# Kernel tuning notes

Measured on AMD Instinct MI355X. Metric: run time of the kernel, lower is better.

Reference implementation:

```python
import jax, jax.numpy as jnp
import numpy as np
from jax import lax

DN = ('NCHW', 'OIHW', 'NCHW')
DENSITY = 0.1  # fraction of active pillar sites


def conv(x, w, stride=1):
    return lax.conv_general_dilated(x, w, (stride, stride), ((1, 1), (1, 1)), dimension_numbers=DN)


def bn(x, s, t):
    # inference-mode BN folded into per-channel scale/shift
    return x * s[None, :, None, None] + t[None, :, None, None]


def subm(x, w, s, t, mask):
    # submanifold sparse conv == dense conv on zero-filled grid, outputs kept only at active sites
    return bn(conv(x, w), s, t) * mask


def basic_block(x, mask, w, s, t):
    # Sparse2DBasicBlock: relu(bn(conv)) -> bn(conv) -> add identity -> relu
    out = jax.nn.relu(subm(x, w[0], s[0], t[0], mask))
    out = subm(out, w[1], s[1], t[1], mask)
    return jax.nn.relu(out + x)


def downsample_mask(m):
    # regular sparse conv (k=3, s=2, p=1): output active iff any input in window active
    return lax.reduce_window(m, 0.0, lax.max, (1, 1, 3, 3), (1, 1, 2, 2), ((0, 0), (0, 0), (1, 1), (1, 1)))


def down_stage(x, m_in, wd, w, s, t):
    m = downsample_mask(m_in)
    h = jax.nn.relu(bn(conv(x, wd, 2), s[0], t[0]) * m)
    h = basic_block(h, m, w[0:2], s[1:3], t[1:3])
    h = basic_block(h, m, w[2:4], s[3:5], t[3:5])
    return h, m


def forward_all(x, mask, w1, s1, t1, wd2, w2, s2, t2, wd3, w3, s3, t3, wd4, w4, s4, t4, w5, s5, t5):
    x = x * mask
    # conv1: Sparse2DBasicBlockV (conv0 + block) + Sparse2DBasicBlock
    h = jax.nn.relu(subm(x, w1[0], s1[0], t1[0], mask))
    h = basic_block(h, mask, w1[1:3], s1[1:3], t1[1:3])
    x1 = basic_block(h, mask, w1[3:5], s1[3:5], t1[3:5])
    x2, m2 = down_stage(x1, mask, wd2, w2, s2, t2)
    x3, m3 = down_stage(x2, m2, wd3, w3, s3, t3)
    x4, m4 = down_stage(x3, m3, wd4, w4, s4, t4)
    # conv5: dense stage on x_conv4.dense()
    h = jax.nn.relu(bn(conv(x4, w5[0], 2), s5[0], t5[0]))
    h = jax.nn.relu(bn(conv(h, w5[1]), s5[1], t5[1]))
    x5 = jax.nn.relu(bn(conv(h, w5[2]), s5[2], t5[2]))
    return x1, x2, x3, x4, x5


def setup_inputs() -> dict:
    key = jax.random.key(0)
    ks = jax.random.split(key, 16)
    B, C, H, W = 2, 32, 512, 512

    def mkw(k, o, i, n=None):
        shape = (o, i, 3, 3) if n is None else (n, o, i, 3, 3)
        return jax.random.normal(k, shape, jnp.float32) * float(np.sqrt(2.0 / (i * 9)))

    def sb(k, n, c):
        k1, k2 = jax.random.split(k)
        return (1.0 + 0.1 * jax.random.normal(k1, (n, c), jnp.float32),
                0.05 * jax.random.normal(k2, (n, c), jnp.float32))

    x = jax.random.normal(ks[0], (B, C, H, W), jnp.float32)
    mask_p = jax.random.uniform(ks[1], (B, 1, H, W), jnp.float32)
    w1 = mkw(ks[2], 32, 32, 5); s1, t1 = sb(ks[3], 5, 32)
    wd2 = mkw(ks[4], 64, 32); w2 = mkw(ks[5], 64, 64, 4); s2, t2 = sb(ks[6], 5, 64)
    wd3 = mkw(ks[7], 128, 64); w3 = mkw(ks[8], 128, 128, 4); s3, t3 = sb(ks[9], 5, 128)
    wd4 = mkw(ks[10], 256, 128); w4 = mkw(ks[11], 256, 256, 4); s4, t4 = sb(ks[12], 5, 256)
    w5 = mkw(ks[13], 256, 256, 3); s5, t5 = sb(ks[14], 3, 256)
    return dict(x=x, mask_p=mask_p, w1=w1, s1=s1, t1=t1, wd2=wd2, w2=w2, s2=s2, t2=t2,
                wd3=wd3, w3=w3, s3=s3, t3=t3, wd4=wd4, w4=w4, s4=s4, t4=t4,
                w5=w5, s5=s5, t5=t5)


def reference(x, mask_p, w1, s1, t1, wd2, w2, s2, t2, wd3, w3, s3, t3, wd4, w4, s4, t4, w5, s5, t5):
    mask = (mask_p < DENSITY).astype(x.dtype)
    return forward_all(x, mask, w1, s1, t1, wd2, w2, s2, t2, wd3, w3, s3, t3, wd4, w4, s4, t4, w5, s5, t5)
```

## Files before the change

### kernel.cpp

```cpp
#include <hip/hip_runtime.h>

typedef __attribute__((ext_vector_type(8))) _Float16 f16x8;
typedef __attribute__((ext_vector_type(4))) _Float16 f16x4;
typedef __attribute__((ext_vector_type(4))) float f32x4;

__global__ void mask_make(const float* __restrict__ x, const float* __restrict__ mp,
                          float* __restrict__ m, _Float16* __restrict__ x0,
                          int* __restrict__ act, int* __restrict__ cnt,
                          int B, int HW) {
    int i = blockIdx.x * blockDim.x + threadIdx.x;
    const int tid = threadIdx.x;
    const int lane = tid & 63;
    const int wv = tid >> 6;
    bool active = (mp[i] < 0.1f);
    float mv = active ? 1.0f : 0.0f;
    m[i] = mv;
    int b = i / HW, p = i - b * HW;
    const float* xb = x + ((size_t)b * 32) * HW + p;
    _Float16* ob = x0 + (size_t)i * 32;
    #pragma unroll
    for (int c = 0; c < 32; ++c) ob[c] = (_Float16)(xb[(size_t)c * HW] * mv);

    __shared__ int wcnt[4];
    __shared__ int bbase;
    unsigned long long ball = __ballot(active);
    int wtot = __popcll(ball);
    int prefix = __popcll(ball & ((1ull << lane) - 1ull));
    if (lane == 0) wcnt[wv] = wtot;
    __syncthreads();
    if (tid == 0) {
        int s = 0;
        #pragma unroll
        for (int w = 0; w < 4; ++w) { int tv = wcnt[w]; wcnt[w] = s; s += tv; }
        bbase = (s > 0) ? atomicAdd(&cnt[b], s) : 0;
    }
    __syncthreads();
    if (active) act[b * HW + bbase + wcnt[wv] + prefix] = p;
}

__global__ void mask_down(const float* __restrict__ mi, float* __restrict__ mo,
                          int B, int Hi, int Wi, int Ho, int Wo) {
    int i = blockIdx.x * blockDim.x + threadIdx.x;
    if (i >= B * Ho * Wo) return;
    int wo = i % Wo;
    int t = i / Wo;
    int ho = t % Ho;
    int b = t / Ho;
    float v = 0.0f;
    #pragma unroll
    for (int kh = 0; kh < 3; ++kh) {
        int hi = ho * 2 + kh - 1;
        if (hi < 0 || hi >= Hi) continue;
        #pragma unroll
        for (int kw = 0; kw < 3; ++kw) {
            int wi = wo * 2 + kw - 1;
            if (wi < 0 || wi >= Wi) continue;
            v = fmaxf(v, mi[((size_t)b * Hi + hi) * Wi + wi]);
        }
    }
    mo[i] = v;
}

struct WSeg { const float* src; int cin, cout, ck, cum; };
struct WArgs { WSeg seg[23]; int total; };

__global__ void reorder_all(WArgs A, _Float16* __restrict__ rw) {
    int idx = blockIdx.x * 256 + threadIdx.x;
    if (idx >= A.total) return;
    int s = 0;
    #pragma unroll
    for (int k = 1; k < 23; ++k) if (idx >= A.seg[k].cum) s = k;
    WSeg g = A.seg[s];
    int local = idx - g.cum;
    int kk = local % g.ck;
    int t2 = local / g.ck;
    int co = t2 % g.cout;
    int chunk = t2 / g.cout;
    int chunkc = g.cin / g.ck;
    int tap = chunk / chunkc, cc = chunk - tap * chunkc;
    int ci = cc * g.ck + kk;
    rw[g.cum + local] = (_Float16)g.src[((size_t)co * g.cin + ci) * 9 + tap];
}

template<int BM, int BN, int CK>
__global__ __launch_bounds__(256, 4)
void conv_mfma(const _Float16* __restrict__ in, const _Float16* __restrict__ rw,
               const float* __restrict__ s, const float* __restrict__ t,
               const float* __restrict__ mask, const _Float16* __restrict__ res,
               float* __restrict__ out32, _Float16* __restrict__ out16,
               int Cin, int Cout, int Hin, int Win, int Hout, int Wout,
               int TH, int TW, int stride, int relu)
{
    constexpr int WM = BM / 2;
    constexpr int WAVES_N = 2;
    constexpr int WN = BN / WAVES_N;
    constexpr int MR = WM / 16;
    constexpr int NR = WN / 16;
    constexpr int KH = CK / 32;
    constexpr int ELEMS = (CK * BN) / 256;
    constexpr int NV = ELEMS / 8;
    constexpr int TPP = 256 / BN;
    constexpr int LDST = CK + 8;

    __shared__ _Float16 Bsm[2][BN * LDST];

    const int tid = threadIdx.x;
    const int lane = tid & 63;
    const int wv = tid >> 6;
    const int wm = wv >> 1;
    const int wn = wv & 1;
    const int row = lane & 15, q = lane >> 4;

    const int tilesX = Wout / TW;
    const int oy0 = (blockIdx.x / tilesX) * TH;
    const int ox0 = (blockIdx.x % tilesX) * TW;
    const int co0 = blockIdx.y * BM;
    const int b = blockIdx.z;

    const int HWin = Hin * Win;
    const int HWo = Hout * Wout;
    const int cicn = Cin >> 5;
    const int cocn = Cout >> 5;
    const int chunkc = Cin / CK;
    const int nIter = 9 * chunkc;

    const int sn = tid / TPP;
    const int kb = (tid % TPP) * ELEMS;
    const int sty = sn / TW;
    const int stx = sn - sty * TW;
    const int soy = oy0 + sty;
    const int sox = ox0 + stx;

    f32x4 acc[MR][NR];
    #pragma unroll
    for (int m = 0; m < MR; ++m)
        #pragma unroll
        for (int n = 0; n < NR; ++n)
            #pragma unroll
            for (int r = 0; r < 4; ++r) acc[m][n][r] = 0.0f;

    auto LOADG = [&](int c, f16x8* dst) {
        int tap = c / chunkc, cc = c - tap * chunkc;
        int iy = soy * stride + (tap / 3) - 1;
        int ix = sox * stride + (tap - (tap / 3) * 3) - 1;
        bool ok = (iy >= 0 && iy < Hin && ix >= 0 && ix < Win);
        size_t pixoff = (size_t)iy * Win + ix;
        #pragma unroll
        for (int i = 0; i < NV; ++i) {
            int k = kb + 8 * i;
            const _Float16* p = in +
                (((size_t)(b * cicn + cc * KH + (k >> 5)) * HWin + pixoff) << 5) + (k & 31);
            dst[i] = ok ? *(const f16x8*)p : f16x8{};
        }
    };
    auto LOADW = [&](int c, f16x8 (&dst)[KH][MR]) {
        #pragma unroll
        for (int m = 0; m < MR; ++m) {
            int co = co0 + wm * WM + m * 16 + row;
            const _Float16* ap = rw + ((size_t)c * Cout + co) * CK + (q << 3);
            #pragma unroll
            for (int h = 0; h < KH; ++h) dst[h][m] = *(const f16x8*)(ap + 32 * h);
        }
    };
    auto WLDS = [&](int buf, const f16x8* v) {
        #pragma unroll
        for (int i = 0; i < NV; ++i)
            *(f16x8*)&Bsm[buf][sn * LDST + kb + 8 * i] = v[i];
    };
    auto DO_CHUNK = [&](const _Float16* bp, f16x8 (&awx)[KH][MR]) {
        f16x8 bh[KH][NR];
        #pragma unroll
        for (int n = 0; n < NR; ++n) {
            int nl = wn * WN + n * 16 + row;
            const _Float16* bb = bp + nl * LDST + (q << 3);
            #pragma unroll
            for (int h = 0; h < KH; ++h) bh[h][n] = *(const f16x8*)(bb + 32 * h);
        }
        #pragma unroll
        for (int h = 0; h < KH; ++h)
            #pragma unroll
            for (int m = 0; m < MR; ++m)
                #pragma unroll
                for (int n = 0; n < NR; ++n)
                    acc[m][n] = __builtin_amdgcn_mfma_f32_16x16x32_f16(awx[h][m], bh[h][n], acc[m][n], 0, 0, 0);
    };

    f16x8 awA[KH][MR], awB[KH][MR];
    f16x8 v[NV];
    LOADG(0, v);
    LOADW(0, awA);
    WLDS(0, v);
    __syncthreads();

    for (int c = 0; c < nIter; c += 2) {
        f16x8 v2[NV];
        bool h1 = (c + 1) < nIter;
        if (h1) { LOADG(c + 1, v2); LOADW(c + 1, awB); }
        DO_CHUNK(&Bsm[0][0], awA);
        if (h1) WLDS(1, v2);
        __syncthreads();
        if (!h1) break;
        f16x8 v3[NV];
        bool h2 = (c + 2) < nIter;
        if (h2) { LOADG(c + 2, v3); LOADW(c + 2, awA); }
        DO_CHUNK(&Bsm[1][0], awB);
        if (h2) WLDS(0, v3);
        __syncthreads();
    }

    int pix[NR]; float mv[NR];
    #pragma unroll
    for (int n = 0; n < NR; ++n) {
        int nl = wn * WN + n * 16 + row;
        int ty = nl / TW, tx = nl - ty * TW;
        pix[n] = (oy0 + ty) * Wout + (ox0 + tx);
        mv[n] = mask ? mask[(size_t)b * HWo + pix[n]] : 1.0f;
    }
    #pragma unroll
    for (int m = 0; m < MR; ++m) {
        int cb = co0 + wm * WM + m * 16 + q * 4;
        float sc[4], sh[4];
        #pragma unroll
        for (int r = 0; r < 4; ++r) { sc[r] = s[cb + r]; sh[r] = t[cb + r]; }
        #pragma unroll
        for (int n = 0; n < NR; ++n) {
            size_t boff = ((size_t)(b * cocn + (cb >> 5)) * HWo + pix[n]) * 32 + (cb & 31);
            float val[4];
            #pragma unroll
            for (int r = 0; r < 4; ++r) val[r] = (acc[m][n][r] * sc[r] + sh[r]) * mv[n];
            if (res) {
                f16x4 rv = *(const f16x4*)&res[boff];
                #pragma unroll
                for (int r = 0; r < 4; ++r) val[r] += (float)rv[r];
            }
            if (relu) {
                #pragma unroll
                for (int r = 0; r < 4; ++r) val[r] = fmaxf(val[r], 0.0f);
            }
            if (out16) {
                f16x4 pk;
                #pragma unroll
                for (int r = 0; r < 4; ++r) pk[r] = (_Float16)val[r];
                *(f16x4*)&out16[boff] = pk;
            }
            if (out32) {
                #pragma unroll
                for (int r = 0; r < 4; ++r)
                    out32[((size_t)b * Cout + cb + r) * HWo + pix[n]] = val[r];
            }
        }
    }
}

__global__ __launch_bounds__(256, 4)
void conv_bf(const _Float16* __restrict__ in, const _Float16* __restrict__ rw,
             const float* __restrict__ s, const float* __restrict__ t,
             const float* __restrict__ mask, const _Float16* __restrict__ res,
             float* __restrict__ out32, _Float16* __restrict__ out16,
             int Cin, int Cout, int Hin, int Win, int Hout, int Wout,
             int stride, int relu)
{
    const int lane = threadIdx.x & 63;
    const int wv = threadIdx.x >> 6;
    const int row = lane & 15, q = lane >> 4;
    const int b = blockIdx.z;
    const int HWo = Hout * Wout;
    const int ntile = HWo >> 4;
    const int gw = blockIdx.x * 4 + wv;
    const int tile = gw % ntile;
    const int cog = gw / ntile;
    const int co0 = cog * 64;
    const int HWin = Hin * Win;
    const int cicn = Cin >> 5;
    const int cocn = Cout >> 5;
    const int nIter = 9 * cicn;

    const int pix = tile * 16 + row;
    const int py = pix / Wout, px_ = pix - py * Wout;
    const int iy0 = py * stride - 1, ix0 = px_ * stride - 1;
    const _Float16* inb = in + (((size_t)b * cicn) * HWin << 5);

    f32x4 acc[4];
    #pragma unroll
    for (int m = 0; m < 4; ++m)
        #pragma unroll
        for (int r = 0; r < 4; ++r) acc[m][r] = 0.0f;

    auto LOADB = [&](int c, f16x8& dst) {
        int tap = c / cicn, cc = c - tap * cicn;
        int iy = iy0 + tap / 3, ix = ix0 + tap - (tap / 3) * 3;
        bool ok = (iy >= 0 && iy < Hin && ix >= 0 && ix < Win);
        dst = ok ? *(const f16x8*)(inb + (((size_t)cc * HWin + (size_t)iy * Win + ix) << 5) + (q << 3))
                 : f16x8{};
    };
    auto LOADA = [&](int c, f16x8 (&dst)[4]) {
        const _Float16* ap = rw + ((size_t)c * Cout + co0 + row) * 32 + (q << 3);
        #pragma unroll
        for (int m = 0; m < 4; ++m) dst[m] = *(const f16x8*)(ap + (size_t)m * 512);
    };

    f16x8 aA[4], aB[4], bfA, bfB;
    LOADB(0, bfA); LOADA(0, aA);
    for (int c = 0; c < nIter; c += 2) {
        bool h1 = (c + 1) < nIter, h2 = (c + 2) < nIter;
        if (h1) { LOADB(c + 1, bfB); LOADA(c + 1, aB); }
        #pragma unroll
        for (int m = 0; m < 4; ++m)
            acc[m] = __builtin_amdgcn_mfma_f32_16x16x32_f16(aA[m], bfA, acc[m], 0, 0, 0);
        if (h2) { LOADB(c + 2, bfA); LOADA(c + 2, aA); }
        if (h1) {
            #pragma unroll
            for (int m = 0; m < 4; ++m)
                acc[m] = __builtin_amdgcn_mfma_f32_16x16x32_f16(aB[m], bfB, acc[m], 0, 0, 0);
        }
    }

    float mv = mask ? mask[(size_t)b * HWo + pix] : 1.0f;
    #pragma unroll
    for (int m = 0; m < 4; ++m) {
        int cb = co0 + m * 16 + q * 4;
        size_t boff = ((size_t)(b * cocn + (cb >> 5)) * HWo + pix) * 32 + (cb & 31);
        float val[4];
        #pragma unroll
        for (int r = 0; r < 4; ++r) val[r] = (acc[m][r] * s[cb + r] + t[cb + r]) * mv;
        if (res) {
            f16x4 rv = *(const f16x4*)&res[boff];
            #pragma unroll
            for (int r = 0; r < 4; ++r) val[r] += (float)rv[r];
        }
        if (relu) {
            #pragma unroll
            for (int r = 0; r < 4; ++r) val[r] = fmaxf(val[r], 0.0f);
        }
        if (out16) {
            f16x4 pk;
            #pragma unroll
            for (int r = 0; r < 4; ++r) pk[r] = (_Float16)val[r];
            *(f16x4*)&out16[boff] = pk;
        }
        if (out32) {
            #pragma unroll
            for (int r = 0; r < 4; ++r)
                out32[((size_t)b * Cout + cb + r) * HWo + pix] = val[r];
        }
    }
}

__global__ __launch_bounds__(256, 4)
void conv_sparse(const _Float16* __restrict__ in, const _Float16* __restrict__ rw,
                 const float* __restrict__ s, const float* __restrict__ t,
                 const int* __restrict__ act, const int* __restrict__ cnt,
                 const _Float16* __restrict__ res,
                 float* __restrict__ out32, _Float16* __restrict__ out16,
                 int Hin, int Win, int relu)
{
    const int tid = threadIdx.x;
    const int lane = tid & 63;
    const int wv = tid >> 6;
    const int row = lane & 15, q = lane >> 4;
    const int b = blockIdx.z;
    const int HW = Hin * Win;
    const int nb = cnt[b];
    const int base = (blockIdx.x * 4 + wv) * 16;
    if (base >= nb) return;

    const int* actb = act + b * HW;
    const _Float16* inb = in + ((size_t)b * HW << 5);

    int j = base + row;
    bool vn = j < nb;
    int pn = vn ? actb[j] : 0;
    int py = pn / Win, px = pn - py * Win;

    f32x4 acc0, acc1;
    #pragma unroll
    for (int r = 0; r < 4; ++r) { acc0[r] = 0.0f; acc1[r] = 0.0f; }

    #pragma unroll
    for (int c = 0; c < 9; ++c) {
        const int dy = c / 3 - 1, dx = c - (c / 3) * 3 - 1;
        f16x8 a0 = *(const f16x8*)(rw + ((size_t)c * 32 + row) * 32 + (q << 3));
        f16x8 a1 = *(const f16x8*)(rw + ((size_t)c * 32 + 16 + row) * 32 + (q << 3));
        int iy = py + dy, ix = px + dx;
        bool ok = vn && iy >= 0 && iy < Hin && ix >= 0 && ix < Win;
        f16x8 bf = ok ? *(const f16x8*)(inb + ((size_t)(iy * Win + ix) << 5) + (q << 3))
                      : f16x8{};
        acc0 = __builtin_amdgcn_mfma_f32_16x16x32_f16(a0, bf, acc0, 0, 0, 0);
        acc1 = __builtin_amdgcn_mfma_f32_16x16x32_f16(a1, bf, acc1, 0, 0, 0);
    }

    if (!vn) return;
    size_t pbase = ((size_t)b * HW + pn) << 5;
    #pragma unroll
    for (int m = 0; m < 2; ++m) {
        const f32x4& am = m ? acc1 : acc0;
        int cb = m * 16 + q * 4;
        float val[4];
        #pragma unroll
        for (int r = 0; r < 4; ++r) val[r] = am[r] * s[cb + r] + t[cb + r];
        if (res) {
            f16x4 rv = *(const f16x4*)&res[pbase + cb];
            #pragma unroll
            for (int r = 0; r < 4; ++r) val[r] += (float)rv[r];
        }
        if (relu) {
            #pragma unroll
            for (int r = 0; r < 4; ++r) val[r] = fmaxf(val[r], 0.0f);
        }
        f16x4 pk;
        #pragma unroll
        for (int r = 0; r < 4; ++r) pk[r] = (_Float16)val[r];
        *(f16x4*)&out16[pbase + cb] = pk;
        if (out32) {
            #pragma unroll
            for (int r = 0; r < 4; ++r)
                out32[((size_t)(b * 32 + cb + r)) * HW + pn] = val[r];
        }
    }
}

extern "C" void kernel_launch(void* const* d_in, const int* in_sizes, int n_in,
                              void* d_out, int out_size, void* d_ws, size_t ws_size,
                              hipStream_t stream) {
    const int B = 2;

    const float* x      = (const float*)d_in[0];
    const float* mask_p = (const float*)d_in[1];
    const float* w1  = (const float*)d_in[2];
    const float* s1  = (const float*)d_in[3];
    const float* t1  = (const float*)d_in[4];
    const float* wd2 = (const float*)d_in[5];
    const float* w2  = (const float*)d_in[6];
    const float* s2  = (const float*)d_in[7];
    const float* t2  = (const float*)d_in[8];
    const float* wd3 = (const float*)d_in[9];
    const float* w3  = (const float*)d_in[10];
    const float* s3  = (const float*)d_in[11];
    const float* t3  = (const float*)d_in[12];
    const float* wd4 = (const float*)d_in[13];
    const float* w4  = (const float*)d_in[14];
    const float* s4  = (const float*)d_in[15];
    const float* t4  = (const float*)d_in[16];
    const float* w5  = (const float*)d_in[17];
    const float* s5  = (const float*)d_in[18];
    const float* t5  = (const float*)d_in[19];

    float* x1o = (float*)d_out;
    float* x2o = x1o + 16777216;
    float* x3o = x2o + 8388608;
    float* x4o = x3o + 4194304;
    float* x5o = x4o + 2097152;

    _Float16* rwbase = (_Float16*)d_ws;
    float* m1 = (float*)d_ws + 2649600;
    float* m2 = m1 + 524288;
    float* m3 = m2 + 131072;
    float* m4 = m3 + 32768;
    int* act  = (int*)(m4 + 8192);
    int* cnt  = act + 524288;
    _Float16* P = (_Float16*)(cnt + 32);
    _Float16* Q = P + 16777216;
    _Float16* R = Q + 16777216;

    WArgs wa;
    int cum = 0, si = 0;
    const _Float16* rp[23];
    auto addseg = [&](const float* src, int cin, int cout, int ck) {
        wa.seg[si].src = src; wa.seg[si].cin = cin; wa.seg[si].cout = cout;
        wa.seg[si].ck = ck; wa.seg[si].cum = cum;
        rp[si] = rwbase + cum;
        cum += cout * cin * 9; si++;
    };
    for (int i = 0; i < 5; ++i) addseg(w1 + (size_t)i * 9216, 32, 32, 32);
    addseg(wd2, 32, 64, 32);
    for (int i = 0; i < 4; ++i) addseg(w2 + (size_t)i * 36864, 64, 64, 64);
    addseg(wd3, 64, 128, 64);
    for (int i = 0; i < 4; ++i) addseg(w3 + (size_t)i * 147456, 128, 128, 64);
    addseg(wd4, 128, 256, 32);
    for (int i = 0; i < 4; ++i) addseg(w4 + (size_t)i * 589824, 256, 256, 32);
    for (int i = 0; i < 3; ++i) addseg(w5 + (size_t)i * 589824, 256, 256, 32);
    wa.total = cum;
    reorder_all<<<(cum + 255) / 256, 256, 0, stream>>>(wa, rwbase);

    hipMemsetAsync(cnt, 0, 2 * sizeof(int), stream);
    hipMemsetAsync(Q, 0, 2 * 16777216 * sizeof(_Float16), stream);
    hipMemsetAsync(x1o, 0, 16777216 * sizeof(float), stream);

    {
        int n = B * 512 * 512;
        mask_make<<<(n + 255) / 256, 256, 0, stream>>>(x, mask_p, m1, P, act, cnt, B, 512 * 512);
        mask_down<<<(B * 256 * 256 + 255) / 256, 256, 0, stream>>>(m1, m2, B, 512, 512, 256, 256);
        mask_down<<<(B * 128 * 128 + 255) / 256, 256, 0, stream>>>(m2, m3, B, 256, 256, 128, 128);
        mask_down<<<(B * 64 * 64 + 255) / 256, 256, 0, stream>>>(m3, m4, B, 128, 128, 64, 64);
    }

    auto conv = [&](const _Float16* in, const _Float16* rwp, const float* sp, const float* tp,
                    const float* mk, const _Float16* rs, float* o32, _Float16* o16,
                    int Cin, int Cout, int Hin, int Win, int stride, int CK) {
        int Hout = Hin / stride, Wout = Win / stride, HWo = Hout * Wout;
        int TW = (Wout < 64) ? Wout : 64;
        int TH = 64 / TW;
        dim3 grid(HWo / 64, Cout / 64, B);
        if (CK == 32)
            conv_mfma<64, 64, 32><<<grid, 256, 0, stream>>>(in, rwp, sp, tp, mk, rs, o32, o16,
                Cin, Cout, Hin, Win, Hout, Wout, TH, TW, stride, 1);
        else
            conv_mfma<64, 64, 64><<<grid, 256, 0, stream>>>(in, rwp, sp, tp, mk, rs, o32, o16,
                Cin, Cout, Hin, Win, Hout, Wout, TH, TW, stride, 1);
    };
    auto bconv = [&](const _Float16* in, const _Float16* rwp, const float* sp, const float* tp,
                     const float* mk, const _Float16* rs, float* o32, _Float16* o16,
                     int Cin, int Cout, int Hin, int Win, int stride) {
        int Hout = Hin / stride, Wout = Win / stride, HWo = Hout * Wout;
        int waves = (HWo / 16) * (Cout / 64);
        dim3 grid(waves / 4, 1, B);
        conv_bf<<<grid, 256, 0, stream>>>(in, rwp, sp, tp, mk, rs, o32, o16,
            Cin, Cout, Hin, Win, Hout, Wout, stride, 1);
    };
    auto sconv = [&](const _Float16* in, const _Float16* rwp, const float* sp, const float* tp,
                     const _Float16* rs, float* o32, _Float16* o16) {
        dim3 grid(1024, 1, B);
        conv_sparse<<<grid, 256, 0, stream>>>(in, rwp, sp, tp, act, cnt, rs, o32, o16, 512, 512, 1);
    };

    sconv(P, rp[0], s1 + 0,   t1 + 0,   nullptr, nullptr, Q);
    sconv(Q, rp[1], s1 + 32,  t1 + 32,  nullptr, nullptr, R);
    sconv(R, rp[2], s1 + 64,  t1 + 64,  Q,       nullptr, P);
    sconv(P, rp[3], s1 + 96,  t1 + 96,  nullptr, nullptr, Q);
    sconv(Q, rp[4], s1 + 128, t1 + 128, P,       x1o,     R);

    conv(R, rp[5], s2 + 0,   t2 + 0,   m2, nullptr, nullptr, P, 32, 64, 512, 512, 2, 32);
    conv(P, rp[6], s2 + 64,  t2 + 64,  m2, nullptr, nullptr, Q, 64, 64, 256, 256, 1, 64);
    conv(Q, rp[7], s2 + 128, t2 + 128, m2, P,       nullptr, P, 64, 64, 256, 256, 1, 64);
    conv(P, rp[8], s2 + 192, t2 + 192, m2, nullptr, nullptr, Q, 64, 64, 256, 256, 1, 64);
    conv(Q, rp[9], s2 + 256, t2 + 256, m2, P,       x2o,     P, 64, 64, 256, 256, 1, 64);

    conv(P, rp[10], s3 + 0,   t3 + 0,   m3, nullptr, nullptr, Q, 64, 128, 256, 256, 2, 64);
    conv(Q, rp[11], s3 + 128, t3 + 128, m3, nullptr, nullptr, R, 128, 128, 128, 128, 1, 64);
    conv(R, rp[12], s3 + 256, t3 + 256, m3, Q,       nullptr, Q, 128, 128, 128, 128, 1, 64);
    conv(Q, rp[13], s3 + 384, t3 + 384, m3, nullptr, nullptr, R, 128, 128, 128, 128, 1, 64);
    conv(R, rp[14], s3 + 512, t3 + 512, m3, Q,       x3o,     Q, 128, 128, 128, 128, 1, 64);

    bconv(Q, rp[15], s4 + 0,    t4 + 0,    m4, nullptr, nullptr, P, 128, 256, 128, 128, 2);
    bconv(P, rp[16], s4 + 256,  t4 + 256,  m4, nullptr, nullptr, R, 256, 256, 64, 64, 1);
    bconv(R, rp[17], s4 + 512,  t4 + 512,  m4, P,       nullptr, P, 256, 256, 64, 64, 1);
    bconv(P, rp[18], s4 + 768,  t4 + 768,  m4, nullptr, nullptr, R, 256, 256, 64, 64, 1);
    bconv(R, rp[19], s4 + 1024, t4 + 1024, m4, P,       x4o,     P, 256, 256, 64, 64, 1);

    bconv(P, rp[20], s5 + 0,   t5 + 0,   nullptr, nullptr, nullptr, Q, 256, 256, 64, 64, 2);
    bconv(Q, rp[21], s5 + 256, t5 + 256, nullptr, nullptr, nullptr, R, 256, 256, 32, 32, 1);
    bconv(R, rp[22], s5 + 512, t5 + 512, nullptr, nullptr, x5o, nullptr, 256, 256, 32, 32, 1);
}
```

Baseline: 1.086 ms.

## Add halo-tiled conv kernel staging 8x8 input patches in LDS for stride-1 stages

Adds a conv_halo kernel that loads a 10x10 halo patch covering all input channels into shared memory (XOR-swizzled) once per 8x8 output tile, then runs all 9 taps from LDS with double-buffered weight loads. The kernel is used for the stride-1 convs in stages 2 and 3, replacing the im2col-style conv_mfma path. All weights are now reordered with a 32-channel chunk so one layout serves every kernel. The aim is to stop re-fetching overlapping input pixels for each tap. In exchange, each block computes only 64 pixels by 64 output channels, and larger LDS use may limit occupancy.

```diff
diff --git a/kernel.cpp b/kernel.cpp
--- a/kernel.cpp
+++ b/kernel.cpp
@@ -224,6 +224,148 @@
         for (int r = 0; r < 4; ++r) { sc[r] = s[cb + r]; sh[r] = t[cb + r]; }
         #pragma unroll
         for (int n = 0; n < NR; ++n) {
+            size_t boff = ((size_t)(b * cocn + (cb >> 5)) * HWo + pix[n]) * 32 + (cb & 31);
+            float val[4];
+            #pragma unroll
+            for (int r = 0; r < 4; ++r) val[r] = (acc[m][n][r] * sc[r] + sh[r]) * mv[n];
+            if (res) {
+                f16x4 rv = *(const f16x4*)&res[boff];
+                #pragma unroll
+                for (int r = 0; r < 4; ++r) val[r] += (float)rv[r];
+            }
+            if (relu) {
+                #pragma unroll
+                for (int r = 0; r < 4; ++r) val[r] = fmaxf(val[r], 0.0f);
+            }
+            if (out16) {
+                f16x4 pk;
+                #pragma unroll
+                for (int r = 0; r < 4; ++r) pk[r] = (_Float16)val[r];
+                *(f16x4*)&out16[boff] = pk;
+            }
+            if (out32) {
+                #pragma unroll
+                for (int r = 0; r < 4; ++r)
+                    out32[((size_t)b * Cout + cb + r) * HWo + pix[n]] = val[r];
+            }
+        }
+    }
+}
+
+template<int CIN>
+__global__ __launch_bounds__(256, 4)
+void conv_halo(const _Float16* __restrict__ in, const _Float16* __restrict__ rw,
+               const float* __restrict__ s, const float* __restrict__ t,
+               const float* __restrict__ mask, const _Float16* __restrict__ res,
+               float* __restrict__ out32, _Float16* __restrict__ out16,
+               int Cout, int Hin, int Win,
+               int relu)
+{
+    constexpr int CV = CIN / 8;
+    constexpr int NPIX = 100;
+    constexpr int NI = 9 * (CIN / 32);
+    constexpr int TOT = NPIX * CV;
+
+    __shared__ _Float16 Bsm[NPIX * CIN];
+
+    const int tid = threadIdx.x;
+    const int lane = tid & 63;
+    const int wv = tid >> 6;
+    const int wm = wv >> 1;
+    const int wn = wv & 1;
+    const int row = lane & 15, q = lane >> 4;
+
+    const int Wout = Win, Hout = Hin;
+    const int tilesX = Wout >> 3;
+    const int oy0 = (blockIdx.x / tilesX) << 3;
+    const int ox0 = (blockIdx.x % tilesX) << 3;
+    const int co0 = blockIdx.y * 64;
+    const int b = blockIdx.z;
+
+    const int HWin = Hin * Win;
+    const int cicn = CIN >> 5;
+    const int cocn = Cout >> 5;
+
+    #pragma unroll
+    for (int l = 0; l < (TOT + 255) / 256; ++l) {
+        int idx = tid + l * 256;
+        if (idx < TOT) {
+            int hp = idx / CV, v = idx - hp * CV;
+            int hy = oy0 - 1 + hp / 10;
+            int hx = ox0 - 1 + hp % 10;
+            bool ok = (hy >= 0 && hy < Hin && hx >= 0 && hx < Win);
+            f16x8 val = f16x8{};
+            if (ok) {
+                const _Float16* p = in +
+                    (((size_t)(b * cicn + (v >> 2)) * HWin + (size_t)hy * Win + hx) << 5) + ((v & 3) << 3);
+                val = *(const f16x8*)p;
+            }
+            int sw = v ^ (hp & 7);
+            *(f16x8*)&Bsm[hp * CIN + (sw << 3)] = val;
+        }
+    }
+    __syncthreads();
+
+    f32x4 acc[2][2];
+    #pragma unroll
+    for (int m = 0; m < 2; ++m)
+        #pragma unroll
+        for (int n = 0; n < 2; ++n)
+            #pragma unroll
+            for (int r = 0; r < 4; ++r) acc[m][n][r] = 0.0f;
+
+    auto LOADW = [&](int c, f16x8 (&dst)[2]) {
+        #pragma unroll
+        for (int m = 0; m < 2; ++m) {
+            int co = co0 + wm * 32 + m * 16 + row;
+            dst[m] = *(const f16x8*)(rw + ((size_t)c * Cout + co) * 32 + (q << 3));
+        }
+    };
+
+    int ty[2], tx[2];
+    #pragma unroll
+    for (int n = 0; n < 2; ++n) {
+        int nl = wn * 32 + n * 16 + row;
+        ty[n] = nl >> 3; tx[n] = nl & 7;
+    }
+
+    f16x8 awA[2], awB[2];
+    LOADW(0, awA);
+    #pragma unroll
+    for (int c = 0; c < NI; ++c) {
+        if (c + 1 < NI) LOADW(c + 1, (c & 1) ? awA : awB);
+        const f16x8* aw = (c & 1) ? awB : awA;
+        const int tap = c / (CIN / 32), cc = c % (CIN / 32);
+        const int dy = tap / 3, dx = tap - dy * 3;
+        f16x8 bh[2];
+        #pragma unroll
+        for (int n = 0; n < 2; ++n) {
+            int hp = (ty[n] + dy) * 10 + tx[n] + dx;
+            int slot = ((cc << 2) + q) ^ (hp & 7);
+            bh[n] = *(const f16x8*)&Bsm[hp * CIN + (slot << 3)];
+        }
+        #pragma unroll
+        for (int m = 0; m < 2; ++m)
+            #pragma unroll
+            for (int n = 0; n < 2; ++n)
+                acc[m][n] = __builtin_amdgcn_mfma_f32_16x16x32_f16(aw[m], bh[n], acc[m][n], 0, 0, 0);
+    }
+
+    const int HWo = Hout * Wout;
+    int pix[2]; float mv[2];
+    #pragma unroll
+    for (int n = 0; n < 2; ++n) {
+        pix[n] = (oy0 + ty[n]) * Wout + (ox0 + tx[n]);
+        mv[n] = mask ? mask[(size_t)b * HWo + pix[n]] : 1.0f;
+    }
+    #pragma unroll
+    for (int m = 0; m < 2; ++m) {
+        int cb = co0 + wm * 32 + m * 16 + q * 4;
+        float sc[4], sh[4];
+        #pragma unroll
+        for (int r = 0; r < 4; ++r) { sc[r] = s[cb + r]; sh[r] = t[cb + r]; }
+        #pragma unroll
+        for (int n = 0; n < 2; ++n) {
             size_t boff = ((size_t)(b * cocn + (cb >> 5)) * HWo + pix[n]) * 32 + (cb & 31);
             float val[4];
             #pragma unroll
@@ -465,20 +607,20 @@
     WArgs wa;
     int cum = 0, si = 0;
     const _Float16* rp[23];
-    auto addseg = [&](const float* src, int cin, int cout, int ck) {
+    auto addseg = [&](const float* src, int cin, int cout) {
         wa.seg[si].src = src; wa.seg[si].cin = cin; wa.seg[si].cout = cout;
-        wa.seg[si].ck = ck; wa.seg[si].cum = cum;
+        wa.seg[si].ck = 32; wa.seg[si].cum = cum;
         rp[si] = rwbase + cum;
         cum += cout * cin * 9; si++;
     };
-    for (int i = 0; i < 5; ++i) addseg(w1 + (size_t)i * 9216, 32, 32, 32);
-    addseg(wd2, 32, 64, 32);
-    for (int i = 0; i < 4; ++i) addseg(w2 + (size_t)i * 36864, 64, 64, 64);
-    addseg(wd3, 64, 128, 64);
-    for (int i = 0; i < 4; ++i) addseg(w3 + (size_t)i * 147456, 128, 128, 64);
-    addseg(wd4, 128, 256, 32);
-    for (int i = 0; i < 4; ++i) addseg(w4 + (size_t)i * 589824, 256, 256, 32);
-    for (int i = 0; i < 3; ++i) addseg(w5 + (size_t)i * 589824, 256, 256, 32);
+    for (int i = 0; i < 5; ++i) addseg(w1 + (size_t)i * 9216, 32, 32);
+    addseg(wd2, 32, 64);
+    for (int i = 0; i < 4; ++i) addseg(w2 + (size_t)i * 36864, 64, 64);
+    addseg(wd3, 64, 128);
+    for (int i = 0; i < 4; ++i) addseg(w3 + (size_t)i * 147456, 128, 128);
+    addseg(wd4, 128, 256);
+    for (int i = 0; i < 4; ++i) addseg(w4 + (size_t)i * 589824, 256, 256);
+    for (int i = 0; i < 3; ++i) addseg(w5 + (size_t)i * 589824, 256, 256);
     wa.total = cum;
     reorder_all<<<(cum + 255) / 256, 256, 0, stream>>>(wa, rwbase);
 
@@ -496,17 +638,24 @@
 
     auto conv = [&](const _Float16* in, const _Float16* rwp, const float* sp, const float* tp,
                     const float* mk, const _Float16* rs, float* o32, _Float16* o16,
-                    int Cin, int Cout, int Hin, int Win, int stride, int CK) {
+                    int Cin, int Cout, int Hin, int Win, int stride) {
         int Hout = Hin / stride, Wout = Win / stride, HWo = Hout * Wout;
         int TW = (Wout < 64) ? Wout : 64;
         int TH = 64 / TW;
         dim3 grid(HWo / 64, Cout / 64, B);
-        if (CK == 32)
-            conv_mfma<64, 64, 32><<<grid, 256, 0, stream>>>(in, rwp, sp, tp, mk, rs, o32, o16,
-                Cin, Cout, Hin, Win, Hout, Wout, TH, TW, stride, 1);
+        conv_mfma<64, 64, 32><<<grid, 256, 0, stream>>>(in, rwp, sp, tp, mk, rs, o32, o16,
+            Cin, Cout, Hin, Win, Hout, Wout, TH, TW, stride, 1);
+    };
+    auto hconv = [&](const _Float16* in, const _Float16* rwp, const float* sp, const float* tp,
+                     const float* mk, const _Float16* rs, float* o32, _Float16* o16,
+                     int Cin, int Cout, int Hin, int Win) {
+        dim3 grid((Hin / 8) * (Win / 8), Cout / 64, B);
+        if (Cin == 64)
+            conv_halo<64><<<grid, 256, 0, stream>>>(in, rwp, sp, tp, mk, rs, o32, o16,
+                Cout, Hin, Win, 1);
         else
-            conv_mfma<64, 64, 64><<<grid, 256, 0, stream>>>(in, rwp, sp, tp, mk, rs, o32, o16,
-                Cin, Cout, Hin, Win, Hout, Wout, TH, TW, stride, 1);
+            conv_halo<128><<<grid, 256, 0, stream>>>(in, rwp, sp, tp, mk, rs, o32, o16,
+                Cout, Hin, Win, 1);
     };
     auto bconv = [&](const _Float16* in, const _Float16* rwp, const float* sp, const float* tp,
                      const float* mk, const _Float16* rs, float* o32, _Float16* o16,
@@ -529,17 +678,17 @@
     sconv(P, rp[3], s1 + 96,  t1 + 96,  nullptr, nullptr, Q);
     sconv(Q, rp[4], s1 + 128, t1 + 128, P,       x1o,     R);
 
-    conv(R, rp[5], s2 + 0,   t2 + 0,   m2, nullptr, nullptr, P, 32, 64, 512, 512, 2, 32);
-    conv(P, rp[6], s2 + 64,  t2 + 64,  m2, nullptr, nullptr, Q, 64, 64, 256, 256, 1, 64);
-    conv(Q, rp[7], s2 + 128, t2 + 128, m2, P,       nullptr, P, 64, 64, 256, 256, 1, 64);
-    conv(P, rp[8], s2 + 192, t2 + 192, m2, nullptr, nullptr, Q, 64, 64, 256, 256, 1, 64);
-    conv(Q, rp[9], s2 + 256, t2 + 256, m2, P,       x2o,     P, 64, 64, 256, 256, 1, 64);
-
-    conv(P, rp[10], s3 + 0,   t3 + 0,   m3, nullptr, nullptr, Q, 64, 128, 256, 256, 2, 64);
-    conv(Q, rp[11], s3 + 128, t3 + 128, m3, nullptr, nullptr, R, 128, 128, 128, 128, 1, 64);
-    conv(R, rp[12], s3 + 256, t3 + 256, m3, Q,       nullptr, Q, 128, 128, 128, 128, 1, 64);
-    conv(Q, rp[13], s3 + 384, t3 + 384, m3, nullptr, nullptr, R, 128, 128, 128, 128, 1, 64);
-    conv(R, rp[14], s3 + 512, t3 + 512, m3, Q,       x3o,     Q, 128, 128, 128, 128, 1, 64);
+    conv (R, rp[5], s2 + 0,   t2 + 0,   m2, nullptr, nullptr, P, 32, 64, 512, 512, 2);
+    hconv(P, rp[6], s2 + 64,  t2 + 64,  m2, nullptr, nullptr, Q, 64, 64, 256, 256);
+    hconv(Q, rp[7], s2 + 128, t2 + 128, m2, P,       nullptr, P, 64, 64, 256, 256);
+    hconv(P, rp[8], s2 + 192, t2 + 192, m2, nullptr, nullptr, Q, 64, 64, 256, 256);
+    hconv(Q, rp[9], s2 + 256, t2 + 256, m2, P,       x2o,     P, 64, 64, 256, 256);
+
+    conv (P, rp[10], s3 + 0,   t3 + 0,   m3, nullptr, nullptr, Q, 64, 128, 256, 256, 2);
+    hconv(Q, rp[11], s3 + 128, t3 + 128, m3, nullptr, nullptr, R, 128, 128, 128, 128);
+    hconv(R, rp[12], s3 + 256, t3 + 256, m3, Q,       nullptr, Q, 128, 128, 128, 128);
+    hconv(Q, rp[13], s3 + 384, t3 + 384, m3, nullptr, nullptr, R, 128, 128, 128, 128);
+    hconv(R, rp[14], s3 + 512, t3 + 512, m3, Q,       x3o,     Q, 128, 128, 128, 128);
 
     bconv(Q, rp[15], s4 + 0,    t4 + 0,    m4, nullptr, nullptr, P, 128, 256, 128, 128, 2);
     bconv(P, rp[16], s4 + 256,  t4 + 256,  m4, nullptr, nullptr, R, 256, 256, 64, 64, 1);
```

Result: faster. 928.1 us (-14.6%).
